# Performance work log

Measured on AMD Instinct MI355X. Metric: run time of the kernel, lower is better.

## Reference

```python
import jax, jax.numpy as jnp
import numpy as np


def _level(cs, bp, i, ih, iw):
    """Process one FPN level.
    cs: (B, 6, h, w) class scores; bp: (B, 12, h, w) bbox deltas; i: level index (2..6).
    Returns scores (B, 3hw, 2), decoded boxes (B, 3hw, 4), anchors (B, 3hw, 4).
    """
    B, _, h, w = bp.shape
    cs = cs.reshape(B, 3, 2, h, w).transpose(0, 1, 3, 4, 2).reshape(B, 3 * h * w, 2)
    bp = bp.reshape(B, 3, 4, h, w).transpose(0, 1, 3, 4, 2).reshape(B, 3 * h * w, 4)

    # enlarge_coord applied i times: c -> 2^i * c + 0.5*(2^i - 1)
    s = 2.0 ** i
    cy = s * jnp.arange(h, dtype=jnp.float32) + 0.5 * (s - 1.0)
    cx = s * jnp.arange(w, dtype=jnp.float32) + 0.5 * (s - 1.0)

    ha = float(ih) / 2 ** (6 - i)
    wa = float(iw) / 2 ** (6 - i)
    # three aspect-ratio anchors: (ha, 2wa), (ha, wa), (2ha, wa)
    hs = jnp.array([ha, ha, 2.0 * ha], dtype=jnp.float32)
    ws = jnp.array([2.0 * wa, wa, wa], dtype=jnp.float32)

    a_cy = jnp.broadcast_to(cy[None, :, None], (3, h, w))
    a_cx = jnp.broadcast_to(cx[None, None, :], (3, h, w))
    a_h = jnp.broadcast_to(hs[:, None, None], (3, h, w))
    a_w = jnp.broadcast_to(ws[:, None, None], (3, h, w))
    anchors = jnp.stack([a_cy, a_cx, a_h, a_w], axis=-1).reshape(1, 3 * h * w, 4)
    anchors = jnp.broadcast_to(anchors, (B, 3 * h * w, 4))

    # apply_deltas
    cyc = anchors[..., 0] + bp[..., 0] * anchors[..., 2]
    cxc = anchors[..., 1] + bp[..., 1] * anchors[..., 3]
    hh = anchors[..., 2] * jnp.exp(bp[..., 2])
    ww = anchors[..., 3] * jnp.exp(bp[..., 3])
    fih, fiw = float(ih), float(iw)
    y1 = jnp.clip(cyc - 0.5 * hh, 0.0, fih)
    x1 = jnp.clip(cxc - 0.5 * ww, 0.0, fiw)
    y2 = jnp.clip(cyc + 0.5 * hh, 0.0, fih)
    x2 = jnp.clip(cxc + 0.5 * ww, 0.0, fiw)
    boxes = jnp.stack([y1, x1, y2, x2], axis=-1)
    return cs, boxes, anchors


def setup_inputs() -> dict:
    key = jax.random.key(0)
    B, IH, IW = 16, 1024, 1024
    ks = jax.random.split(key, 10)
    d = {}
    for idx, i in enumerate(range(2, 7)):
        h, w = IH // 2 ** i, IW // 2 ** i
        d[f"cs{i}"] = jax.random.normal(ks[2 * idx], (B, 6, h, w), dtype=jnp.float32)
        d[f"bp{i}"] = jax.random.normal(ks[2 * idx + 1], (B, 12, h, w), dtype=jnp.float32)
    d["img_h"] = IH
    d["img_w"] = IW
    return d


def reference(cs2, cs3, cs4, cs5, cs6, bp2, bp3, bp4, bp5, bp6, img_h, img_w):
    css = (cs2, cs3, cs4, cs5, cs6)
    bps = (bp2, bp3, bp4, bp5, bp6)
    scoress, bboxess, anchorss = [], [], []
    for idx, i in enumerate(range(2, 7)):
        s, b, a = _level(css[idx], bps[idx], i, img_h, img_w)
        scoress.append(s)
        bboxess.append(b)
        anchorss.append(a)
    return (jnp.concatenate(scoress, axis=1),
            jnp.concatenate(bboxess, axis=1),
            jnp.concatenate(anchorss, axis=1))
```

## Files before the change

kernel.cpp:

```cpp
#include <hip/hip_runtime.h>
#include <math.h>


#define BATCH 16
#define NPOS  261888
#define N4    (NPOS / 4)

__global__ __launch_bounds__(256) void fpn_decode_kernel(
    const float* __restrict__ cs2, const float* __restrict__ bp2,
    const float* __restrict__ cs3, const float* __restrict__ bp3,
    const float* __restrict__ cs4, const float* __restrict__ bp4,
    const float* __restrict__ cs5, const float* __restrict__ bp5,
    const float* __restrict__ cs6, const float* __restrict__ bp6,
    float* __restrict__ out)
{
    const int g = blockIdx.x * blockDim.x + threadIdx.x;
    if (g >= BATCH * N4) return;

    const int b  = g / N4;
    const int m4 = g - b * N4;
    const int n  = m4 * 4;

    const float* cs; const float* bp;
    int off, lgw, lghw; float scale, coff, ah0;
    if (n < 196608)      { cs=cs2; bp=bp2; off=0;      lgw=8; lghw=16; scale=4.f;  coff=1.5f;  ah0=64.f;   }
    else if (n < 245760) { cs=cs3; bp=bp3; off=196608; lgw=7; lghw=14; scale=8.f;  coff=3.5f;  ah0=128.f;  }
    else if (n < 258048) { cs=cs4; bp=bp4; off=245760; lgw=6; lghw=12; scale=16.f; coff=7.5f;  ah0=256.f;  }
    else if (n < 261120) { cs=cs5; bp=bp5; off=258048; lgw=5; lghw=10; scale=32.f; coff=15.5f; ah0=512.f;  }
    else                 { cs=cs6; bp=bp6; off=261120; lgw=4; lghw=8;  scale=64.f; coff=31.5f; ah0=1024.f; }

    const int m  = n - off;
    const int hw = 1 << lghw;
    const int a  = m >> lghw;
    const int r  = m & (hw - 1);
    const int y  = r >> lgw;
    const int x  = r & ((1 << lgw) - 1);

    const float ah = (a == 2) ? 2.f * ah0 : ah0;
    const float aw = (a == 0) ? 2.f * ah0 : ah0;

    const float cy  = scale * (float)y + coff;
    const float cx0 = scale * (float)x + coff;

    const size_t csbase = ((size_t)(b * 6  + 2 * a)) * hw + r;
    const size_t bpbase = ((size_t)(b * 12 + 4 * a)) * hw + r;
    const float4 c0 = *(const float4*)(cs + csbase);
    const float4 c1 = *(const float4*)(cs + csbase + hw);
    const float4 d0 = *(const float4*)(bp + bpbase);
    const float4 d1 = *(const float4*)(bp + bpbase + (size_t)hw);
    const float4 d2 = *(const float4*)(bp + bpbase + 2 * (size_t)hw);
    const float4 d3 = *(const float4*)(bp + bpbase + 3 * (size_t)hw);

    const size_t sidx = ((size_t)b * NPOS + n) * 2;
    *(float4*)(out + sidx)     = make_float4(c0.x, c1.x, c0.y, c1.y);
    *(float4*)(out + sidx + 4) = make_float4(c0.z, c1.z, c0.w, c1.w);

    float* const bx = out + (size_t)BATCH * NPOS * 2;
    float* const an = out + (size_t)BATCH * NPOS * 6;
    const size_t bidx = ((size_t)b * NPOS + n) * 4;

    const float FIH = 1024.f, FIW = 1024.f;

#define DECODE_ONE(J, DY, DX, DH, DW)                                        \
    {                                                                        \
        const float cxj = cx0 + scale * (float)(J);                          \
        const float cyc = cy  + (DY) * ah;                                   \
        const float cxc = cxj + (DX) * aw;                                   \
        const float hh  = ah * expf(DH);                                     \
        const float ww  = aw * expf(DW);                                     \
        const float y1 = fminf(fmaxf(cyc - 0.5f * hh, 0.f), FIH);            \
        const float x1 = fminf(fmaxf(cxc - 0.5f * ww, 0.f), FIW);            \
        const float y2 = fminf(fmaxf(cyc + 0.5f * hh, 0.f), FIH);            \
        const float x2 = fminf(fmaxf(cxc + 0.5f * ww, 0.f), FIW);            \
        *(float4*)(bx + bidx + 4 * (J)) = make_float4(y1, x1, y2, x2);       \
        *(float4*)(an + bidx + 4 * (J)) = make_float4(cy, cxj, ah, aw);      \
    }

    DECODE_ONE(0, d0.x, d1.x, d2.x, d3.x)
    DECODE_ONE(1, d0.y, d1.y, d2.y, d3.y)
    DECODE_ONE(2, d0.z, d1.z, d2.z, d3.z)
    DECODE_ONE(3, d0.w, d1.w, d2.w, d3.w)
#undef DECODE_ONE
}

extern "C" void kernel_launch(void* const* d_in, const int* in_sizes, int n_in,
                              void* d_out, int out_size, void* d_ws, size_t ws_size,
                              hipStream_t stream) {
    const float* cs2 = (const float*)d_in[0];
    const float* bp2 = (const float*)d_in[1];
    const float* cs3 = (const float*)d_in[2];
    const float* bp3 = (const float*)d_in[3];
    const float* cs4 = (const float*)d_in[4];
    const float* bp4 = (const float*)d_in[5];
    const float* cs5 = (const float*)d_in[6];
    const float* bp5 = (const float*)d_in[7];
    const float* cs6 = (const float*)d_in[8];
    const float* bp6 = (const float*)d_in[9];
    float* out = (float*)d_out;

    const int total = BATCH * N4;
    const dim3 block(256);
    const dim3 grid((total + 255) / 256);
    hipLaunchKernelGGL(fpn_decode_kernel, grid, block, 0, stream,
                       cs2, bp2, cs3, bp3, cs4, bp4, cs5, bp5, cs6, bp6, out);
}
```

Measured before the change: 273.7 us.

## Stage outputs through shared memory for fully coalesced stores

Each block now handles 1024 contiguous positions. Scores and decoded boxes are staged in padded LDS buffers and then written back with lane-contiguous float4 stores, so stores are no longer strided per thread. Anchors are recomputed per position in the store phase, and expf is replaced with __expf. The cost is an added barrier, extra LDS traffic and occupancy limited by LDS use, plus slightly lower exp precision.

```diff
diff --git a/kernel.cpp b/kernel.cpp
--- a/kernel.cpp
+++ b/kernel.cpp
@@ -4,9 +4,20 @@
 
 #define BATCH 16
 #define NPOS  261888
-#define N4    (NPOS / 4)
+#define TOTAL (BATCH * NPOS)
+#define PPB   1024
+#define NBLK  (TOTAL / PPB)
 
-__global__ __launch_bounds__(256) void fpn_decode_kernel(
+__device__ __forceinline__ void level_params(int n, int& off, int& lgw, int& lghw,
+                                             float& scale, float& coff, float& ah0) {
+    if (n < 196608)      { off = 0;      lgw = 8; lghw = 16; scale = 4.f;  coff = 1.5f;  ah0 = 64.f;   }
+    else if (n < 245760) { off = 196608; lgw = 7; lghw = 14; scale = 8.f;  coff = 3.5f;  ah0 = 128.f;  }
+    else if (n < 258048) { off = 245760; lgw = 6; lghw = 12; scale = 16.f; coff = 7.5f;  ah0 = 256.f;  }
+    else if (n < 261120) { off = 258048; lgw = 5; lghw = 10; scale = 32.f; coff = 15.5f; ah0 = 512.f;  }
+    else                 { off = 261120; lgw = 4; lghw = 8;  scale = 64.f; coff = 31.5f; ah0 = 1024.f; }
+}
+
+__global__ __launch_bounds__(256, 4) void fpn_decode_kernel(
     const float* __restrict__ cs2, const float* __restrict__ bp2,
     const float* __restrict__ cs3, const float* __restrict__ bp3,
     const float* __restrict__ cs4, const float* __restrict__ bp4,
@@ -14,73 +25,117 @@
     const float* __restrict__ cs6, const float* __restrict__ bp6,
     float* __restrict__ out)
 {
-    const int g = blockIdx.x * blockDim.x + threadIdx.x;
-    if (g >= BATCH * N4) return;
+    __shared__ __align__(16) float s_sc[256 * 12];
+    __shared__ __align__(16) float s_bx[256 * 20];
 
-    const int b  = g / N4;
-    const int m4 = g - b * N4;
-    const int n  = m4 * 4;
+    const int t  = threadIdx.x;
+    const int P0 = blockIdx.x * PPB;
 
-    const float* cs; const float* bp;
-    int off, lgw, lghw; float scale, coff, ah0;
-    if (n < 196608)      { cs=cs2; bp=bp2; off=0;      lgw=8; lghw=16; scale=4.f;  coff=1.5f;  ah0=64.f;   }
-    else if (n < 245760) { cs=cs3; bp=bp3; off=196608; lgw=7; lghw=14; scale=8.f;  coff=3.5f;  ah0=128.f;  }
-    else if (n < 258048) { cs=cs4; bp=bp4; off=245760; lgw=6; lghw=12; scale=16.f; coff=7.5f;  ah0=256.f;  }
-    else if (n < 261120) { cs=cs5; bp=bp5; off=258048; lgw=5; lghw=10; scale=32.f; coff=15.5f; ah0=512.f;  }
-    else                 { cs=cs6; bp=bp6; off=261120; lgw=4; lghw=8;  scale=64.f; coff=31.5f; ah0=1024.f; }
+    {
+        const int P = P0 + 4 * t;
+        const int b = P / NPOS;
+        const int n = P - b * NPOS;
 
-    const int m  = n - off;
-    const int hw = 1 << lghw;
-    const int a  = m >> lghw;
-    const int r  = m & (hw - 1);
-    const int y  = r >> lgw;
-    const int x  = r & ((1 << lgw) - 1);
+        int off, lgw, lghw; float scale, coff, ah0;
+        level_params(n, off, lgw, lghw, scale, coff, ah0);
+        const float* cs; const float* bp;
+        if (n < 196608)      { cs = cs2; bp = bp2; }
+        else if (n < 245760) { cs = cs3; bp = bp3; }
+        else if (n < 258048) { cs = cs4; bp = bp4; }
+        else if (n < 261120) { cs = cs5; bp = bp5; }
+        else                 { cs = cs6; bp = bp6; }
 
-    const float ah = (a == 2) ? 2.f * ah0 : ah0;
-    const float aw = (a == 0) ? 2.f * ah0 : ah0;
+        const int m  = n - off;
+        const int hw = 1 << lghw;
+        const int a  = m >> lghw;
+        const int r  = m & (hw - 1);
+        const int y  = r >> lgw;
+        const int x  = r & ((1 << lgw) - 1);
 
-    const float cy  = scale * (float)y + coff;
-    const float cx0 = scale * (float)x + coff;
+        const float ah = (a == 2) ? 2.f * ah0 : ah0;
+        const float aw = (a == 0) ? 2.f * ah0 : ah0;
+        const float cy  = scale * (float)y + coff;
+        const float cx0 = scale * (float)x + coff;
 
-    const size_t csbase = ((size_t)(b * 6  + 2 * a)) * hw + r;
-    const size_t bpbase = ((size_t)(b * 12 + 4 * a)) * hw + r;
-    const float4 c0 = *(const float4*)(cs + csbase);
-    const float4 c1 = *(const float4*)(cs + csbase + hw);
-    const float4 d0 = *(const float4*)(bp + bpbase);
-    const float4 d1 = *(const float4*)(bp + bpbase + (size_t)hw);
-    const float4 d2 = *(const float4*)(bp + bpbase + 2 * (size_t)hw);
-    const float4 d3 = *(const float4*)(bp + bpbase + 3 * (size_t)hw);
+        const size_t csbase = ((size_t)(b * 6  + 2 * a)) * hw + r;
+        const size_t bpbase = ((size_t)(b * 12 + 4 * a)) * hw + r;
+        const float4 c0 = *(const float4*)(cs + csbase);
+        const float4 c1 = *(const float4*)(cs + csbase + hw);
+        const float4 d0 = *(const float4*)(bp + bpbase);
+        const float4 d1 = *(const float4*)(bp + bpbase + (size_t)hw);
+        const float4 d2 = *(const float4*)(bp + bpbase + 2 * (size_t)hw);
+        const float4 d3 = *(const float4*)(bp + bpbase + 3 * (size_t)hw);
 
-    const size_t sidx = ((size_t)b * NPOS + n) * 2;
-    *(float4*)(out + sidx)     = make_float4(c0.x, c1.x, c0.y, c1.y);
-    *(float4*)(out + sidx + 4) = make_float4(c0.z, c1.z, c0.w, c1.w);
+        float4* sc = (float4*)&s_sc[12 * t];
+        sc[0] = make_float4(c0.x, c1.x, c0.y, c1.y);
+        sc[1] = make_float4(c0.z, c1.z, c0.w, c1.w);
 
-    float* const bx = out + (size_t)BATCH * NPOS * 2;
-    float* const an = out + (size_t)BATCH * NPOS * 6;
-    const size_t bidx = ((size_t)b * NPOS + n) * 4;
-
-    const float FIH = 1024.f, FIW = 1024.f;
-
+        float4* bxl = (float4*)&s_bx[20 * t];
+        const float FIH = 1024.f, FIW = 1024.f;
 #define DECODE_ONE(J, DY, DX, DH, DW)                                        \
-    {                                                                        \
-        const float cxj = cx0 + scale * (float)(J);                          \
-        const float cyc = cy  + (DY) * ah;                                   \
-        const float cxc = cxj + (DX) * aw;                                   \
-        const float hh  = ah * expf(DH);                                     \
-        const float ww  = aw * expf(DW);                                     \
-        const float y1 = fminf(fmaxf(cyc - 0.5f * hh, 0.f), FIH);            \
-        const float x1 = fminf(fmaxf(cxc - 0.5f * ww, 0.f), FIW);            \
-        const float y2 = fminf(fmaxf(cyc + 0.5f * hh, 0.f), FIH);            \
-        const float x2 = fminf(fmaxf(cxc + 0.5f * ww, 0.f), FIW);            \
-        *(float4*)(bx + bidx + 4 * (J)) = make_float4(y1, x1, y2, x2);       \
-        *(float4*)(an + bidx + 4 * (J)) = make_float4(cy, cxj, ah, aw);      \
+        {                                                                    \
+            const float cxj = cx0 + scale * (float)(J);                      \
+            const float cyc = cy  + (DY) * ah;                               \
+            const float cxc = cxj + (DX) * aw;                               \
+            const float hh  = ah * __expf(DH);                               \
+            const float ww  = aw * __expf(DW);                               \
+            const float y1 = fminf(fmaxf(cyc - 0.5f * hh, 0.f), FIH);        \
+            const float x1 = fminf(fmaxf(cxc - 0.5f * ww, 0.f), FIW);        \
+            const float y2 = fminf(fmaxf(cyc + 0.5f * hh, 0.f), FIH);        \
+            const float x2 = fminf(fmaxf(cxc + 0.5f * ww, 0.f), FIW);        \
+            bxl[J] = make_float4(y1, x1, y2, x2);                            \
+        }
+        DECODE_ONE(0, d0.x, d1.x, d2.x, d3.x)
+        DECODE_ONE(1, d0.y, d1.y, d2.y, d3.y)
+        DECODE_ONE(2, d0.z, d1.z, d2.z, d3.z)
+        DECODE_ONE(3, d0.w, d1.w, d2.w, d3.w)
+#undef DECODE_ONE
     }
 
-    DECODE_ONE(0, d0.x, d1.x, d2.x, d3.x)
-    DECODE_ONE(1, d0.y, d1.y, d2.y, d3.y)
-    DECODE_ONE(2, d0.z, d1.z, d2.z, d3.z)
-    DECODE_ONE(3, d0.w, d1.w, d2.w, d3.w)
-#undef DECODE_ONE
+    __syncthreads();
+
+    {
+        float* so = out + (size_t)2 * P0;
+#pragma unroll
+        for (int j = 0; j < 2; ++j) {
+            const int f = 1024 * j + 4 * t;
+            const int q = f >> 1;
+            const int c = q >> 2;
+            const int w = 12 * c + 2 * (q & 3);
+            *(float4*)(so + f) = *(const float4*)&s_sc[w];
+        }
+    }
+    {
+        float* bo = out + (size_t)TOTAL * 2 + (size_t)4 * P0;
+#pragma unroll
+        for (int j = 0; j < 4; ++j) {
+            const int q = 256 * j + t;
+            const int w = 20 * (q >> 2) + 4 * (q & 3);
+            *(float4*)(bo + 4 * q) = *(const float4*)&s_bx[w];
+        }
+    }
+    {
+        float* ao = out + (size_t)TOTAL * 6 + (size_t)4 * P0;
+#pragma unroll
+        for (int j = 0; j < 4; ++j) {
+            const int q = 256 * j + t;
+            const int P = P0 + q;
+            const int b = P / NPOS;
+            const int n = P - b * NPOS;
+            int off, lgw, lghw; float scale, coff, ah0;
+            level_params(n, off, lgw, lghw, scale, coff, ah0);
+            const int m = n - off;
+            const int a = m >> lghw;
+            const int r = m & ((1 << lghw) - 1);
+            const int y = r >> lgw;
+            const int x = r & ((1 << lgw) - 1);
+            const float ah = (a == 2) ? 2.f * ah0 : ah0;
+            const float aw = (a == 0) ? 2.f * ah0 : ah0;
+            const float cy = scale * (float)y + coff;
+            const float cx = scale * (float)x + coff;
+            *(float4*)(ao + 4 * q) = make_float4(cy, cx, ah, aw);
+        }
+    }
 }
 
 extern "C" void kernel_launch(void* const* d_in, const int* in_sizes, int n_in,
@@ -98,9 +153,8 @@
     const float* bp6 = (const float*)d_in[9];
     float* out = (float*)d_out;
 
-    const int total = BATCH * N4;
     const dim3 block(256);
-    const dim3 grid((total + 255) / 256);
+    const dim3 grid(NBLK);
     hipLaunchKernelGGL(fpn_decode_kernel, grid, block, 0, stream,
                        cs2, bp2, cs3, bp3, cs4, bp4, cs5, bp5, cs6, bp6, out);
 }
```

New measurement: 261.1 us. 4.6% less time.
